# Optimization experiments

Hardware: AMD Instinct MI355X
Metric: run time of the kernel (lower is better)

The kernel has to match this reference:

```python
import jax, jax.numpy as jnp
import numpy as np

B, S, D = 2, 2048, 2048
KVH, QPG, HD = 8, 4, 64          # kv heads, q heads per group, head size
THETA = 1024.0
PARTIAL = 0.5
SOFT_CAP = 50.0
EPS = 1e-5


def setup_inputs() -> dict:
    key = jax.random.key(0)
    ks = jax.random.split(key, 8)
    scale = 0.02
    return {
        "x": jax.random.normal(ks[0], (B, S, D), jnp.float32),
        "wq": jax.random.normal(ks[1], (KVH, QPG, HD, D), jnp.float32) * scale,
        "wk": jax.random.normal(ks[2], (KVH, HD, D), jnp.float32) * scale,
        "wv": jax.random.normal(ks[3], (KVH, HD, D), jnp.float32) * scale,
        "wo": jax.random.normal(ks[4], (D, KVH, QPG, HD), jnp.float32) * scale,
        "qn_w": jnp.ones((HD,), jnp.float32),
        "kn_w": jnp.ones((HD,), jnp.float32),
        "pos_ids": jnp.arange(S, dtype=jnp.int32),
    }


def _rms_norm(t, w):
    var = jnp.mean(jnp.square(t), axis=-1, keepdims=True)
    return t * jax.lax.rsqrt(var + EPS) * w


def _rope_tables(pos_ids):
    half = HD // 2
    rotated_size = int(HD * PARTIAL)
    inv_freq = 1.0 / THETA ** (jnp.arange(0, 2 * half, 2, dtype=jnp.float32) / rotated_size)
    inv_freq = jnp.where(jnp.arange(half) < rotated_size // 2, inv_freq, 0.0)
    freqs = pos_ids.astype(jnp.float32)[:, None] * inv_freq[None, :]   # [S, half]
    emb = jnp.concatenate([freqs, freqs], axis=-1)                      # [S, HD]
    return jnp.cos(emb), jnp.sin(emb)


def _apply_rope(t, cos, sin):
    # t: [..., S, HD]; rotate_half: (x1, x2) -> (-x2, x1)
    half = HD // 2
    x1, x2 = t[..., :half], t[..., half:]
    rot = jnp.concatenate([-x2, x1], axis=-1)
    return t * cos + rot * sin


def reference(x, wq, wk, wv, wo, qn_w, kn_w, pos_ids):
    # QKV projections (GQA)
    q = jnp.einsum("bsd,gphd->bgpsh", x, wq)   # [B,KVH,QPG,S,HD]
    k = jnp.einsum("bsd,ghd->bgsh", x, wk)      # [B,KVH,S,HD]
    v = jnp.einsum("bsd,ghd->bgsh", x, wv)

    # QK-norm (RMS over head dim)
    q = _rms_norm(q, qn_w)
    k = _rms_norm(k, kn_w)

    # partial RoPE
    cos, sin = _rope_tables(pos_ids)            # [S, HD]
    q = _apply_rope(q, cos, sin).astype(x.dtype)
    k = _apply_rope(k, cos, sin).astype(x.dtype)

    # attention in fp32 (upcast_attn) with soft cap and causal mask
    scale = 1.0 / jnp.sqrt(jnp.float32(HD))
    scores = jnp.einsum("bgpsh,bgth->bgpst", q.astype(jnp.float32), k.astype(jnp.float32)) * scale
    scores = SOFT_CAP * jnp.tanh(scores / SOFT_CAP)
    causal = pos_ids[:, None] >= pos_ids[None, :]                    # [S, S]
    scores = jnp.where(causal, scores, jnp.finfo(jnp.float32).min)
    probs = jax.nn.softmax(scores, axis=-1)
    attn = jnp.einsum("bgpst,bgth->bgpsh", probs, v.astype(jnp.float32)).astype(x.dtype)

    # output projection (flatten kv_head x q_heads_per_group -> heads)
    out = jnp.einsum("bgpsh,dgph->bsd", attn, wo)
    return out
```

## Files before the change

kernel.cpp:

```cpp
#include <hip/hip_runtime.h>
#include <stdint.h>

#define S_LEN   2048
#define D_MODEL 2048
#define N_KVH   8
#define N_QPG   4
#define N_HD    64

typedef __attribute__((ext_vector_type(8))) short  short8;
typedef __attribute__((ext_vector_type(4))) short  short4v;
typedef __attribute__((ext_vector_type(4))) float  float4v;

__device__ __forceinline__ unsigned short f2bf(float x) {
    unsigned int u = __float_as_uint(x);
    u = (u + 0x7fffu + ((u >> 16) & 1u)) >> 16;
    return (unsigned short)u;
}

__device__ __forceinline__ void gload_lds16(const unsigned short* g, unsigned short* l) {
    __builtin_amdgcn_global_load_lds((const __attribute__((address_space(1))) unsigned int*)g,
                                     (__attribute__((address_space(3))) unsigned int*)l,
                                     16, 0, 0);
}

__device__ __forceinline__ short8 lds_read8(const unsigned short* p) {
    union { short8 s8; short4v s4[2]; } u;
    u.s4[0] = *(const short4v*)p;
    u.s4[1] = *(const short4v*)(p + 4);
    return u.s8;
}

__global__ __launch_bounds__(256) void cvt_all(const float* __restrict__ x,
                                               const float* __restrict__ wq,
                                               const float* __restrict__ wk,
                                               const float* __restrict__ wv,
                                               const float* __restrict__ wo,
                                               unsigned short* __restrict__ xb,
                                               unsigned short* __restrict__ wqb,
                                               unsigned short* __restrict__ wkb,
                                               unsigned short* __restrict__ wvb,
                                               unsigned short* __restrict__ wob) {
    size_t i = (size_t)blockIdx.x * 256 + threadIdx.x;
    const float* src; unsigned short* dst; size_t off;
    if      (i < 1048576) { src = x;  dst = xb;  off = i; }
    else if (i < 1572864) { src = wq; dst = wqb; off = i - 1048576; }
    else if (i < 1703936) { src = wk; dst = wkb; off = i - 1572864; }
    else if (i < 1835008) { src = wv; dst = wvb; off = i - 1703936; }
    else                  { src = wo; dst = wob; off = i - 1835008; }
    const float4* p = (const float4*)src + off * 2;
    float4 a = p[0], b = p[1];
    union { unsigned short us[8]; uint4 v; } u;
    u.us[0] = f2bf(a.x); u.us[1] = f2bf(a.y); u.us[2] = f2bf(a.z); u.us[3] = f2bf(a.w);
    u.us[4] = f2bf(b.x); u.us[5] = f2bf(b.y); u.us[6] = f2bf(b.z); u.us[7] = f2bf(b.w);
    ((uint4*)dst)[off] = u.v;
}

#define EPI_OUT 0
#define EPI_Q   1

template<int EPI>
__global__ __launch_bounds__(256)
void gemm_bt(const unsigned short* __restrict__ A,
             const unsigned short* __restrict__ B,
             void* __restrict__ C,
             const float* __restrict__ normw,
             int M, int N, int K)
{
    __shared__ __align__(16) unsigned short Alds[128 * 32];
    __shared__ __align__(16) unsigned short Blds[128 * 32];

    const int tid  = threadIdx.x;
    const int lane = tid & 63;
    const int wave = tid >> 6;
    const int quad = lane >> 4;
    const int l15  = lane & 15;
    const int m0 = blockIdx.x * 128;
    const int n0 = blockIdx.y * 128;
    const int wm = (wave >> 1) * 64;
    const int wn = (wave & 1) * 64;

    float4v acc[4][4];
#pragma unroll
    for (int i = 0; i < 4; i++)
#pragma unroll
        for (int j = 0; j < 4; j++) acc[i][j] = (float4v){0.f, 0.f, 0.f, 0.f};

    const int j0 = wave * 2;
    const int lr = lane >> 2;
    const int lc = (lane & 3) * 8;
    const unsigned short* Ag = A + (size_t)(m0 + j0 * 16 + lr) * K + lc;
    const unsigned short* Bg = B + (size_t)(n0 + j0 * 16 + lr) * K + lc;
    unsigned short* Al = Alds + j0 * 512;
    unsigned short* Bl = Blds + j0 * 512;

    for (int k0 = 0; k0 < K; k0 += 32) {
        __syncthreads();
        gload_lds16(Ag + k0,          Al);
        gload_lds16(Ag + 16 * K + k0, Al + 512);
        gload_lds16(Bg + k0,          Bl);
        gload_lds16(Bg + 16 * K + k0, Bl + 512);
        __syncthreads();

        short8 af[4], bf[4];
#pragma unroll
        for (int mt = 0; mt < 4; mt++)
            af[mt] = *(const short8*)(Alds + (wm + mt * 16 + l15) * 32 + quad * 8);
#pragma unroll
        for (int nt = 0; nt < 4; nt++)
            bf[nt] = *(const short8*)(Blds + (wn + nt * 16 + l15) * 32 + quad * 8);
#pragma unroll
        for (int mt = 0; mt < 4; mt++)
#pragma unroll
            for (int nt = 0; nt < 4; nt++)
                acc[mt][nt] = __builtin_amdgcn_mfma_f32_16x16x32_bf16(af[mt], bf[nt], acc[mt][nt], 0, 0, 0);
    }

    const int nb = n0 + wn;
#pragma unroll
    for (int mt = 0; mt < 4; mt++) {
#pragma unroll
        for (int r = 0; r < 4; r++) {
            const int m = m0 + wm + mt * 16 + quad * 4 + r;
            if constexpr (EPI == EPI_OUT) {
#pragma unroll
                for (int nt = 0; nt < 4; nt++) {
                    int n = nb + nt * 16 + l15;
                    ((float*)C)[(size_t)m * N + n] = acc[mt][nt][r];
                }
            } else {
                float v0 = acc[mt][0][r], v1 = acc[mt][1][r], v2 = acc[mt][2][r], v3 = acc[mt][3][r];
                float s2 = v0 * v0 + v1 * v1 + v2 * v2 + v3 * v3;
#pragma unroll
                for (int off = 1; off < 16; off <<= 1) s2 += __shfl_xor(s2, off, 64);
                float rs = rsqrtf(s2 * (1.0f / 64.0f) + 1e-5f);
                float nv0 = v0 * rs * normw[0 * 16 + l15];
                float nv1 = v1 * rs * normw[1 * 16 + l15];
                float nv2 = v2 * rs * normw[2 * 16 + l15];
                float nv3 = v3 * rs * normw[3 * 16 + l15];
                const int bidx = m >> 11, s = m & 2047;
                float ang = (float)s * exp2f(-0.625f * (float)l15);
                float sn, cs;
                __sincosf(ang, &sn, &cs);
                float o0 = nv0 * cs - nv2 * sn;
                float o2 = nv2 * cs + nv0 * sn;
                const int g = nb >> 8, p = (nb >> 6) & 3;
                unsigned short* dst = (unsigned short*)C +
                    ((((size_t)bidx * N_KVH + g) * N_QPG + p) * S_LEN + s) * N_HD;
                dst[0 * 16 + l15] = f2bf(o0);
                dst[1 * 16 + l15] = f2bf(nv1);
                dst[2 * 16 + l15] = f2bf(o2);
                dst[3 * 16 + l15] = f2bf(nv3);
            }
        }
    }
}

__global__ __launch_bounds__(256)
void gemm_kv(const unsigned short* __restrict__ xb,
             const unsigned short* __restrict__ wkb,
             const unsigned short* __restrict__ wvb,
             unsigned short* __restrict__ kout,
             unsigned short* __restrict__ vtout,
             const float* __restrict__ knw)
{
    __shared__ __align__(16) unsigned short Alds[128 * 32];
    __shared__ __align__(16) unsigned short Blds[128 * 32];

    const int tid  = threadIdx.x;
    const int lane = tid & 63;
    const int wave = tid >> 6;
    const int quad = lane >> 4;
    const int l15  = lane & 15;
    const int bx = blockIdx.x, by = blockIdx.y;
    const bool isK = (by < 4);
    const unsigned short* A = isK ? xb  : wvb;
    const unsigned short* B = isK ? wkb : xb;
    const int m0 = isK ? bx * 128 : (by - 4) * 128;
    const int n0 = isK ? by * 128 : bx * 128;
    const int K = 2048;
    const int wm = (wave >> 1) * 64;
    const int wn = (wave & 1) * 64;

    float4v acc[4][4];
#pragma unroll
    for (int i = 0; i < 4; i++)
#pragma unroll
        for (int j = 0; j < 4; j++) acc[i][j] = (float4v){0.f, 0.f, 0.f, 0.f};

    const int j0 = wave * 2;
    const int lr = lane >> 2;
    const int lc = (lane & 3) * 8;
    const unsigned short* Ag = A + (size_t)(m0 + j0 * 16 + lr) * K + lc;
    const unsigned short* Bg = B + (size_t)(n0 + j0 * 16 + lr) * K + lc;
    unsigned short* Al = Alds + j0 * 512;
    unsigned short* Bl = Blds + j0 * 512;

    for (int k0 = 0; k0 < K; k0 += 32) {
        __syncthreads();
        gload_lds16(Ag + k0,          Al);
        gload_lds16(Ag + 16 * K + k0, Al + 512);
        gload_lds16(Bg + k0,          Bl);
        gload_lds16(Bg + 16 * K + k0, Bl + 512);
        __syncthreads();

        short8 af[4], bf[4];
#pragma unroll
        for (int mt = 0; mt < 4; mt++)
            af[mt] = *(const short8*)(Alds + (wm + mt * 16 + l15) * 32 + quad * 8);
#pragma unroll
        for (int nt = 0; nt < 4; nt++)
            bf[nt] = *(const short8*)(Blds + (wn + nt * 16 + l15) * 32 + quad * 8);
#pragma unroll
        for (int mt = 0; mt < 4; mt++)
#pragma unroll
            for (int nt = 0; nt < 4; nt++)
                acc[mt][nt] = __builtin_amdgcn_mfma_f32_16x16x32_bf16(af[mt], bf[nt], acc[mt][nt], 0, 0, 0);
    }

    const int nb = n0 + wn;
#pragma unroll
    for (int mt = 0; mt < 4; mt++) {
#pragma unroll
        for (int r = 0; r < 4; r++) {
            const int m = m0 + wm + mt * 16 + quad * 4 + r;
            if (isK) {
                float v0 = acc[mt][0][r], v1 = acc[mt][1][r], v2 = acc[mt][2][r], v3 = acc[mt][3][r];
                float s2 = v0 * v0 + v1 * v1 + v2 * v2 + v3 * v3;
#pragma unroll
                for (int off = 1; off < 16; off <<= 1) s2 += __shfl_xor(s2, off, 64);
                float rs = rsqrtf(s2 * (1.0f / 64.0f) + 1e-5f);
                float nv0 = v0 * rs * knw[0 * 16 + l15];
                float nv1 = v1 * rs * knw[1 * 16 + l15];
                float nv2 = v2 * rs * knw[2 * 16 + l15];
                float nv3 = v3 * rs * knw[3 * 16 + l15];
                const int bidx = m >> 11, s = m & 2047;
                float ang = (float)s * exp2f(-0.625f * (float)l15);
                float sn, cs;
                __sincosf(ang, &sn, &cs);
                float o0 = nv0 * cs - nv2 * sn;
                float o2 = nv2 * cs + nv0 * sn;
                const int g = nb >> 6;
                unsigned short* dst = kout +
                    (((size_t)bidx * N_KVH + g) * S_LEN + s) * N_HD;
                dst[0 * 16 + l15] = f2bf(o0);
                dst[1 * 16 + l15] = f2bf(nv1);
                dst[2 * 16 + l15] = f2bf(o2);
                dst[3 * 16 + l15] = f2bf(nv3);
            } else {
#pragma unroll
                for (int nt = 0; nt < 4; nt++) {
                    int n = nb + nt * 16 + l15;
                    vtout[((size_t)(n >> 11) * 512 + m) * 2048 + (n & 2047)] =
                        f2bf(acc[mt][nt][r]);
                }
            }
        }
    }
}

#define PSTRIDE 68

__global__ __launch_bounds__(256)
void attn_kernel(const unsigned short* __restrict__ Q,
                 const unsigned short* __restrict__ Kb,
                 const unsigned short* __restrict__ Vt,
                 unsigned short* __restrict__ O)
{
    __shared__ __align__(16) unsigned short Plds[4 * 32 * PSTRIDE];

    const int tid  = threadIdx.x;
    const int lane = tid & 63;
    const int w    = tid >> 6;
    const int quad = lane >> 4;
    const int l15  = lane & 15;
    const int qx = blockIdx.y;
    const int bg = blockIdx.x;
    const int b = bg >> 3, g = bg & 7;

    const unsigned short* qbase  = Q  + (((size_t)b * N_KVH + g) * N_QPG + w) * S_LEN * N_HD;
    const unsigned short* kbase  = Kb + ((size_t)b * N_KVH + g) * S_LEN * N_HD;
    const unsigned short* vtbase = Vt + ((size_t)b * N_KVH + g) * (size_t)N_HD * S_LEN;

    unsigned short* Pw = Plds + w * (32 * PSTRIDE);

    for (int half = 0; half < 2; half++) {
        const int qt = half ? (63 - qx) : qx;
        const int qrow0 = qt * 32;

        short8 qf[2][2];
#pragma unroll
        for (int mt = 0; mt < 2; mt++)
#pragma unroll
            for (int ks = 0; ks < 2; ks++)
                qf[mt][ks] = *(const short8*)(qbase + (size_t)(qrow0 + mt * 16 + l15) * N_HD + ks * 32 + quad * 8);

        float4v o_acc[2][4];
#pragma unroll
        for (int mt = 0; mt < 2; mt++)
#pragma unroll
            for (int nt = 0; nt < 4; nt++) o_acc[mt][nt] = (float4v){0.f, 0.f, 0.f, 0.f};
        float rsum[2][4];
#pragma unroll
        for (int mt = 0; mt < 2; mt++)
#pragma unroll
            for (int r = 0; r < 4; r++) rsum[mt][r] = 0.f;

        const int ktend = qrow0 >> 6;

        short8 kf[4][2];
#pragma unroll
        for (int nt = 0; nt < 4; nt++)
#pragma unroll
            for (int ks = 0; ks < 2; ks++)
                kf[nt][ks] = *(const short8*)(kbase + (size_t)(nt * 16 + l15) * N_HD + ks * 32 + quad * 8);

        for (int kt = 0; kt <= ktend; kt++) {
            float4v s_acc[2][4];
#pragma unroll
            for (int mt = 0; mt < 2; mt++)
#pragma unroll
                for (int nt = 0; nt < 4; nt++) s_acc[mt][nt] = (float4v){0.f, 0.f, 0.f, 0.f};
            __builtin_amdgcn_s_setprio(1);
#pragma unroll
            for (int ks = 0; ks < 2; ks++)
#pragma unroll
                for (int mt = 0; mt < 2; mt++)
#pragma unroll
                    for (int nt = 0; nt < 4; nt++)
                        s_acc[mt][nt] = __builtin_amdgcn_mfma_f32_16x16x32_bf16(qf[mt][ks], kf[nt][ks], s_acc[mt][nt], 0, 0, 0);
            __builtin_amdgcn_s_setprio(0);

            short8 vf[4][2];
#pragma unroll
            for (int nt = 0; nt < 4; nt++)
#pragma unroll
                for (int ks = 0; ks < 2; ks++)
                    vf[nt][ks] = *(const short8*)(vtbase + (size_t)(nt * 16 + l15) * S_LEN + kt * 64 + ks * 32 + quad * 8);

            if (kt < ktend) {
#pragma unroll
                for (int nt = 0; nt < 4; nt++)
#pragma unroll
                    for (int ks = 0; ks < 2; ks++)
                        kf[nt][ks] = *(const short8*)(kbase + (size_t)((kt + 1) * 64 + nt * 16 + l15) * N_HD + ks * 32 + quad * 8);
            }

            const bool diag = (kt == ktend);
#pragma unroll
            for (int mt = 0; mt < 2; mt++) {
#pragma unroll
                for (int r = 0; r < 4; r++) {
                    const int s_q  = qrow0 + mt * 16 + quad * 4 + r;
                    const int prow = (mt * 16 + quad * 4 + r) * PSTRIDE;
#pragma unroll
                    for (int nt = 0; nt < 4; nt++) {
                        float a = s_acc[mt][nt][r];
                        float u = a * a;
                        float wv = fmaf(u, -3.757018e-7f, 0.18033688f);
                        float p = __builtin_amdgcn_exp2f(fmaf(a, wv, -72.13475204f));
                        if (diag) {
                            int s_k = kt * 64 + nt * 16 + l15;
                            p = (s_k <= s_q) ? p : 0.0f;
                        }
                        rsum[mt][r] += p;
                        Pw[prow + nt * 16 + l15] =
                            (unsigned short)((__float_as_uint(p) + 0x8000u) >> 16);
                    }
                }
            }

#pragma unroll
            for (int ks = 0; ks < 2; ks++) {
                short8 pf[2];
#pragma unroll
                for (int mt = 0; mt < 2; mt++)
                    pf[mt] = lds_read8(Pw + (mt * 16 + l15) * PSTRIDE + ks * 32 + quad * 8);
                __builtin_amdgcn_s_setprio(1);
#pragma unroll
                for (int mt = 0; mt < 2; mt++)
#pragma unroll
                    for (int nt = 0; nt < 4; nt++)
                        o_acc[mt][nt] = __builtin_amdgcn_mfma_f32_16x16x32_bf16(pf[mt], vf[nt][ks], o_acc[mt][nt], 0, 0, 0);
                __builtin_amdgcn_s_setprio(0);
            }
        }

#pragma unroll
        for (int mt = 0; mt < 2; mt++) {
#pragma unroll
            for (int r = 0; r < 4; r++) {
                float s = rsum[mt][r];
                s += __shfl_xor(s, 1, 64);
                s += __shfl_xor(s, 2, 64);
                s += __shfl_xor(s, 4, 64);
                s += __shfl_xor(s, 8, 64);
                float inv = 1.0f / s;
                int s_q = qrow0 + mt * 16 + quad * 4 + r;
                size_t rowoff = ((size_t)(b * S_LEN + s_q)) * D_MODEL + (g * N_QPG + w) * N_HD;
#pragma unroll
                for (int nt = 0; nt < 4; nt++)
                    O[rowoff + nt * 16 + l15] = f2bf(o_acc[mt][nt][r] * inv);
            }
        }
    }
}

extern "C" void kernel_launch(void* const* d_in, const int* in_sizes, int n_in,
                              void* d_out, int out_size, void* d_ws, size_t ws_size,
                              hipStream_t stream)
{
    const float* x    = (const float*)d_in[0];
    const float* wq   = (const float*)d_in[1];
    const float* wk   = (const float*)d_in[2];
    const float* wv   = (const float*)d_in[3];
    const float* wo   = (const float*)d_in[4];
    const float* qn_w = (const float*)d_in[5];
    const float* kn_w = (const float*)d_in[6];

    char* ws = (char*)d_ws;
    unsigned short* xb  = (unsigned short*)(ws + 0);
    unsigned short* wqb = (unsigned short*)(ws + 16777216);
    unsigned short* wkb = (unsigned short*)(ws + 25165824);
    unsigned short* wvb = (unsigned short*)(ws + 27262976);
    unsigned short* wob = (unsigned short*)(ws + 29360128);
    unsigned short* qb  = (unsigned short*)(ws + 37748736);
    unsigned short* kb  = (unsigned short*)(ws + 54525952);
    unsigned short* vt  = (unsigned short*)(ws + 58720256);
    unsigned short* ab  = (unsigned short*)(ws + 62914560);

    cvt_all<<<dim3(9216), 256, 0, stream>>>(x, wq, wk, wv, wo, xb, wqb, wkb, wvb, wob);

    gemm_bt<EPI_Q><<<dim3(32, 16), 256, 0, stream>>>(xb, wqb, qb, qn_w, 4096, 2048, 2048);
    gemm_kv<<<dim3(32, 8), 256, 0, stream>>>(xb, wkb, wvb, kb, vt, kn_w);

    attn_kernel<<<dim3(16, 32), 256, 0, stream>>>(qb, kb, vt, ab);

    gemm_bt<EPI_OUT><<<dim3(32, 16), 256, 0, stream>>>(ab, wob, d_out, nullptr, 4096, 2048, 2048);
}
```

Baseline: 391.0 us.

## Split attention KV range across two wave groups and merge partials in LDS

Doubles the attention block to 512 threads. The two sets of four waves each process half of the causal KV tiles for the same query tile. Partial outputs and row sums from the second group go to LDS and are added by the first group before normalisation and store. This is safe because softmax uses a fixed max offset. The intent is more parallelism per query tile and more waves in flight to hide latency. The cost is extra LDS for the scratch buffers (about 96KB), two block barriers per half, and uneven splits on short KV ranges.

```diff
diff --git a/kernel.cpp b/kernel.cpp
--- a/kernel.cpp
+++ b/kernel.cpp
@@ -260,32 +260,41 @@
 
 #define PSTRIDE 68
 
-__global__ __launch_bounds__(256)
+__global__ __launch_bounds__(512, 4)
 void attn_kernel(const unsigned short* __restrict__ Q,
                  const unsigned short* __restrict__ Kb,
                  const unsigned short* __restrict__ Vt,
                  unsigned short* __restrict__ O)
 {
-    __shared__ __align__(16) unsigned short Plds[4 * 32 * PSTRIDE];
+    __shared__ __align__(16) unsigned short Plds[8 * 32 * PSTRIDE];
+    __shared__ __align__(16) float4v Osc[8 * 256];
+    __shared__ float Rsc[8 * 256];
 
     const int tid  = threadIdx.x;
     const int lane = tid & 63;
-    const int w    = tid >> 6;
+    const int wv   = tid >> 6;
+    const int p    = wv & 3;
+    const int kvh  = wv >> 2;
     const int quad = lane >> 4;
     const int l15  = lane & 15;
     const int qx = blockIdx.y;
     const int bg = blockIdx.x;
     const int b = bg >> 3, g = bg & 7;
 
-    const unsigned short* qbase  = Q  + (((size_t)b * N_KVH + g) * N_QPG + w) * S_LEN * N_HD;
+    const unsigned short* qbase  = Q  + (((size_t)b * N_KVH + g) * N_QPG + p) * S_LEN * N_HD;
     const unsigned short* kbase  = Kb + ((size_t)b * N_KVH + g) * S_LEN * N_HD;
     const unsigned short* vtbase = Vt + ((size_t)b * N_KVH + g) * (size_t)N_HD * S_LEN;
 
-    unsigned short* Pw = Plds + w * (32 * PSTRIDE);
+    unsigned short* Pw = Plds + wv * (32 * PSTRIDE);
+    const int slot = p * 64 + lane;
 
     for (int half = 0; half < 2; half++) {
         const int qt = half ? (63 - qx) : qx;
         const int qrow0 = qt * 32;
+        const int ktend = qrow0 >> 6;
+        const int nkt = ktend + 1;
+        const int lo = kvh ? (nkt >> 1) : 0;
+        const int hi = kvh ? nkt : (nkt >> 1);
 
         short8 qf[2][2];
 #pragma unroll
@@ -305,101 +314,128 @@
 #pragma unroll
             for (int r = 0; r < 4; r++) rsum[mt][r] = 0.f;
 
-        const int ktend = qrow0 >> 6;
-
-        short8 kf[4][2];
-#pragma unroll
-        for (int nt = 0; nt < 4; nt++)
-#pragma unroll
-            for (int ks = 0; ks < 2; ks++)
-                kf[nt][ks] = *(const short8*)(kbase + (size_t)(nt * 16 + l15) * N_HD + ks * 32 + quad * 8);
-
-        for (int kt = 0; kt <= ktend; kt++) {
-            float4v s_acc[2][4];
-#pragma unroll
-            for (int mt = 0; mt < 2; mt++)
-#pragma unroll
-                for (int nt = 0; nt < 4; nt++) s_acc[mt][nt] = (float4v){0.f, 0.f, 0.f, 0.f};
-            __builtin_amdgcn_s_setprio(1);
-#pragma unroll
-            for (int ks = 0; ks < 2; ks++)
+        if (lo < hi) {
+            short8 kf[4][2];
+#pragma unroll
+            for (int nt = 0; nt < 4; nt++)
+#pragma unroll
+                for (int ks = 0; ks < 2; ks++)
+                    kf[nt][ks] = *(const short8*)(kbase + (size_t)(lo * 64 + nt * 16 + l15) * N_HD + ks * 32 + quad * 8);
+
+            for (int kt = lo; kt < hi; kt++) {
+                float4v s_acc[2][4];
 #pragma unroll
                 for (int mt = 0; mt < 2; mt++)
 #pragma unroll
+                    for (int nt = 0; nt < 4; nt++) s_acc[mt][nt] = (float4v){0.f, 0.f, 0.f, 0.f};
+                __builtin_amdgcn_s_setprio(1);
+#pragma unroll
+                for (int ks = 0; ks < 2; ks++)
+#pragma unroll
+                    for (int mt = 0; mt < 2; mt++)
+#pragma unroll
+                        for (int nt = 0; nt < 4; nt++)
+                            s_acc[mt][nt] = __builtin_amdgcn_mfma_f32_16x16x32_bf16(qf[mt][ks], kf[nt][ks], s_acc[mt][nt], 0, 0, 0);
+                __builtin_amdgcn_s_setprio(0);
+
+                short8 vf[4][2];
+#pragma unroll
+                for (int nt = 0; nt < 4; nt++)
+#pragma unroll
+                    for (int ks = 0; ks < 2; ks++)
+                        vf[nt][ks] = *(const short8*)(vtbase + (size_t)(nt * 16 + l15) * S_LEN + kt * 64 + ks * 32 + quad * 8);
+
+                if (kt + 1 < hi) {
+#pragma unroll
                     for (int nt = 0; nt < 4; nt++)
-                        s_acc[mt][nt] = __builtin_amdgcn_mfma_f32_16x16x32_bf16(qf[mt][ks], kf[nt][ks], s_acc[mt][nt], 0, 0, 0);
-            __builtin_amdgcn_s_setprio(0);
-
-            short8 vf[4][2];
-#pragma unroll
-            for (int nt = 0; nt < 4; nt++)
-#pragma unroll
-                for (int ks = 0; ks < 2; ks++)
-                    vf[nt][ks] = *(const short8*)(vtbase + (size_t)(nt * 16 + l15) * S_LEN + kt * 64 + ks * 32 + quad * 8);
-
-            if (kt < ktend) {
-#pragma unroll
-                for (int nt = 0; nt < 4; nt++)
-#pragma unroll
-                    for (int ks = 0; ks < 2; ks++)
-                        kf[nt][ks] = *(const short8*)(kbase + (size_t)((kt + 1) * 64 + nt * 16 + l15) * N_HD + ks * 32 + quad * 8);
-            }
-
-            const bool diag = (kt == ktend);
-#pragma unroll
-            for (int mt = 0; mt < 2; mt++) {
-#pragma unroll
-                for (int r = 0; r < 4; r++) {
-                    const int s_q  = qrow0 + mt * 16 + quad * 4 + r;
-                    const int prow = (mt * 16 + quad * 4 + r) * PSTRIDE;
-#pragma unroll
-                    for (int nt = 0; nt < 4; nt++) {
-                        float a = s_acc[mt][nt][r];
-                        float u = a * a;
-                        float wv = fmaf(u, -3.757018e-7f, 0.18033688f);
-                        float p = __builtin_amdgcn_exp2f(fmaf(a, wv, -72.13475204f));
-                        if (diag) {
-                            int s_k = kt * 64 + nt * 16 + l15;
-                            p = (s_k <= s_q) ? p : 0.0f;
+#pragma unroll
+                        for (int ks = 0; ks < 2; ks++)
+                            kf[nt][ks] = *(const short8*)(kbase + (size_t)((kt + 1) * 64 + nt * 16 + l15) * N_HD + ks * 32 + quad * 8);
+                }
+
+                const bool diag = (kt == ktend);
+#pragma unroll
+                for (int mt = 0; mt < 2; mt++) {
+#pragma unroll
+                    for (int r = 0; r < 4; r++) {
+                        const int s_q  = qrow0 + mt * 16 + quad * 4 + r;
+                        const int prow = (mt * 16 + quad * 4 + r) * PSTRIDE;
+#pragma unroll
+                        for (int nt = 0; nt < 4; nt++) {
+                            float a = s_acc[mt][nt][r];
+                            float u = a * a;
+                            float wvv = fmaf(u, -3.757018e-7f, 0.18033688f);
+                            float pv = __builtin_amdgcn_exp2f(fmaf(a, wvv, -72.13475204f));
+                            if (diag) {
+                                int s_k = kt * 64 + nt * 16 + l15;
+                                pv = (s_k <= s_q) ? pv : 0.0f;
+                            }
+                            rsum[mt][r] += pv;
+                            Pw[prow + nt * 16 + l15] =
+                                (unsigned short)((__float_as_uint(pv) + 0x8000u) >> 16);
                         }
-                        rsum[mt][r] += p;
-                        Pw[prow + nt * 16 + l15] =
-                            (unsigned short)((__float_as_uint(p) + 0x8000u) >> 16);
                     }
                 }
-            }
-
-#pragma unroll
-            for (int ks = 0; ks < 2; ks++) {
-                short8 pf[2];
-#pragma unroll
-                for (int mt = 0; mt < 2; mt++)
-                    pf[mt] = lds_read8(Pw + (mt * 16 + l15) * PSTRIDE + ks * 32 + quad * 8);
-                __builtin_amdgcn_s_setprio(1);
-#pragma unroll
-                for (int mt = 0; mt < 2; mt++)
-#pragma unroll
-                    for (int nt = 0; nt < 4; nt++)
-                        o_acc[mt][nt] = __builtin_amdgcn_mfma_f32_16x16x32_bf16(pf[mt], vf[nt][ks], o_acc[mt][nt], 0, 0, 0);
-                __builtin_amdgcn_s_setprio(0);
+
+#pragma unroll
+                for (int ks = 0; ks < 2; ks++) {
+                    short8 pf[2];
+#pragma unroll
+                    for (int mt = 0; mt < 2; mt++)
+                        pf[mt] = lds_read8(Pw + (mt * 16 + l15) * PSTRIDE + ks * 32 + quad * 8);
+                    __builtin_amdgcn_s_setprio(1);
+#pragma unroll
+                    for (int mt = 0; mt < 2; mt++)
+#pragma unroll
+                        for (int nt = 0; nt < 4; nt++)
+                            o_acc[mt][nt] = __builtin_amdgcn_mfma_f32_16x16x32_bf16(pf[mt], vf[nt][ks], o_acc[mt][nt], 0, 0, 0);
+                    __builtin_amdgcn_s_setprio(0);
+                }
             }
         }
 
-#pragma unroll
-        for (int mt = 0; mt < 2; mt++) {
-#pragma unroll
-            for (int r = 0; r < 4; r++) {
-                float s = rsum[mt][r];
-                s += __shfl_xor(s, 1, 64);
-                s += __shfl_xor(s, 2, 64);
-                s += __shfl_xor(s, 4, 64);
-                s += __shfl_xor(s, 8, 64);
-                float inv = 1.0f / s;
-                int s_q = qrow0 + mt * 16 + quad * 4 + r;
-                size_t rowoff = ((size_t)(b * S_LEN + s_q)) * D_MODEL + (g * N_QPG + w) * N_HD;
+        __syncthreads();
+        if (kvh == 1) {
+#pragma unroll
+            for (int mt = 0; mt < 2; mt++)
 #pragma unroll
                 for (int nt = 0; nt < 4; nt++)
-                    O[rowoff + nt * 16 + l15] = f2bf(o_acc[mt][nt][r] * inv);
+                    Osc[(mt * 4 + nt) * 256 + slot] = o_acc[mt][nt];
+#pragma unroll
+            for (int mt = 0; mt < 2; mt++)
+#pragma unroll
+                for (int r = 0; r < 4; r++)
+                    Rsc[(mt * 4 + r) * 256 + slot] = rsum[mt][r];
+        }
+        __syncthreads();
+        if (kvh == 0) {
+#pragma unroll
+            for (int mt = 0; mt < 2; mt++)
+#pragma unroll
+                for (int nt = 0; nt < 4; nt++)
+                    o_acc[mt][nt] += Osc[(mt * 4 + nt) * 256 + slot];
+#pragma unroll
+            for (int mt = 0; mt < 2; mt++)
+#pragma unroll
+                for (int r = 0; r < 4; r++)
+                    rsum[mt][r] += Rsc[(mt * 4 + r) * 256 + slot];
+
+#pragma unroll
+            for (int mt = 0; mt < 2; mt++) {
+#pragma unroll
+                for (int r = 0; r < 4; r++) {
+                    float s = rsum[mt][r];
+                    s += __shfl_xor(s, 1, 64);
+                    s += __shfl_xor(s, 2, 64);
+                    s += __shfl_xor(s, 4, 64);
+                    s += __shfl_xor(s, 8, 64);
+                    float inv = 1.0f / s;
+                    int s_q = qrow0 + mt * 16 + quad * 4 + r;
+                    size_t rowoff = ((size_t)(b * S_LEN + s_q)) * D_MODEL + (g * N_QPG + p) * N_HD;
+#pragma unroll
+                    for (int nt = 0; nt < 4; nt++)
+                        O[rowoff + nt * 16 + l15] = f2bf(o_acc[mt][nt][r] * inv);
+                }
             }
         }
     }
@@ -433,7 +469,7 @@
     gemm_bt<EPI_Q><<<dim3(32, 16), 256, 0, stream>>>(xb, wqb, qb, qn_w, 4096, 2048, 2048);
     gemm_kv<<<dim3(32, 8), 256, 0, stream>>>(xb, wkb, wvb, kb, vt, kn_w);
 
-    attn_kernel<<<dim3(16, 32), 256, 0, stream>>>(qb, kb, vt, ab);
+    attn_kernel<<<dim3(16, 32), 512, 0, stream>>>(qb, kb, vt, ab);
 
     gemm_bt<EPI_OUT><<<dim3(32, 16), 256, 0, stream>>>(ab, wob, d_out, nullptr, 4096, 2048, 2048);
 }
```

After: 570.1 us. +45.8%, slower.
